# Optimization experiments

Hardware: AMD Instinct MI355X
Metric: run time of the kernel (lower is better)

## Reference

```python
import jax, jax.numpy as jnp
import numpy as np

N = 50000
NEG_SLOPE = 0.2  # PyG GATConv default leaky_relu slope


def _gat_layer(x, src, dst, W, a_s, a_d, b):
    # x: [N, Fin]; W: [Fin, H*C]; a_s, a_d: [H, C]; b: [C]
    H, C = a_s.shape
    xp = (x @ W).reshape(N, H, C)                      # projected node features per head
    alpha_s = jnp.einsum('nhc,hc->nh', xp, a_s)        # [N, H]
    alpha_d = jnp.einsum('nhc,hc->nh', xp, a_d)        # [N, H]
    e = jax.nn.leaky_relu(alpha_s[src] + alpha_d[dst], NEG_SLOPE)  # [E, H]
    # segment softmax over incoming edges of each dst node
    m = jax.ops.segment_max(e, dst, num_segments=N)
    m = jnp.where(jnp.isfinite(m), m, 0.0)
    p = jnp.exp(e - jax.lax.stop_gradient(m)[dst])
    denom = jax.ops.segment_sum(p, dst, num_segments=N)
    alpha = p / denom[dst]                             # [E, H]
    # scatter-aggregate messages
    out = jax.ops.segment_sum(alpha[:, :, None] * xp[src], dst, num_segments=N)  # [N, H, C]
    return out.mean(axis=1) + b                        # concat=False -> mean over heads


def setup_inputs() -> dict:
    key = jax.random.key(0)
    ks = jax.random.split(key, 16)
    IN, HID, OUT, H = 128, 64, 40, 4
    E = 800000
    x = jax.random.normal(ks[0], (N, IN), dtype=jnp.float32)
    edge_index = jax.random.randint(ks[1], (2, E), 0, N, dtype=jnp.int64)

    def mk(kw, ka, fin, fout):
        s = 1.0 / np.sqrt(fin)
        W = jax.random.normal(kw, (fin, H * fout), dtype=jnp.float32) * s
        a_s = jax.random.normal(ka, (H, fout), dtype=jnp.float32) * 0.1
        a_d = jax.random.normal(jax.random.fold_in(ka, 1), (H, fout), dtype=jnp.float32) * 0.1
        b = jnp.zeros((fout,), dtype=jnp.float32)
        return W, a_s, a_d, b

    W1, as1, ad1, b1 = mk(ks[2], ks[3], IN, HID)
    W2, as2, ad2, b2 = mk(ks[4], ks[5], HID, HID)
    W3, as3, ad3, b3 = mk(ks[6], ks[7], HID, OUT)
    return dict(x=x, edge_index=edge_index,
                W1=W1, as1=as1, ad1=ad1, b1=b1,
                W2=W2, as2=as2, ad2=ad2, b2=b2,
                W3=W3, as3=as3, ad3=ad3, b3=b3)


def reference(x, edge_index, W1, as1, ad1, b1, W2, as2, ad2, b2, W3, as3, ad3, b3):
    # PyG GATConv adds self-loops by default
    loop = jnp.arange(N, dtype=edge_index.dtype)
    src = jnp.concatenate([edge_index[0], loop])
    dst = jnp.concatenate([edge_index[1], loop])
    h = jax.nn.relu(_gat_layer(x, src, dst, W1, as1, ad1, b1))   # dropout is identity in eval
    h = jax.nn.relu(_gat_layer(h, src, dst, W2, as2, ad2, b2))
    h = jax.nn.relu(_gat_layer(h, src, dst, W3, as3, ad3, b3))
    return jax.nn.log_softmax(h, axis=-1)
```

## Files before the change

kernel.cpp:

```cpp
#include <hip/hip_runtime.h>
#include <math.h>

#define NNODES 50000
#define NEG_SLOPE 0.2f

typedef unsigned short ushort8v __attribute__((ext_vector_type(8)));
typedef unsigned short ushort4v __attribute__((ext_vector_type(4)));
typedef short short8v __attribute__((ext_vector_type(8)));
typedef float f32x4 __attribute__((ext_vector_type(4)));

__device__ __forceinline__ float lrelu(float x){ return x > 0.f ? x : NEG_SLOPE * x; }
__device__ __forceinline__ float bf2f(unsigned short u){ return __uint_as_float(((unsigned)u) << 16); }
__device__ __forceinline__ unsigned short f2bf(float f){
    unsigned u = __float_as_uint(f);
    u += 0x7fff + ((u >> 16) & 1);
    return (unsigned short)(u >> 16);
}

__global__ void detect_kernel(const unsigned long long* __restrict__ e, int* __restrict__ flag){
    const unsigned long long v = e[threadIdx.x & 63];
    const unsigned long long mask = __ballot(v >= (1ULL << 32));
    if(threadIdx.x == 0) *flag = (mask == 0ULL) ? 1 : 0;
}

__global__ void convert_kernel(const void* __restrict__ e, const int* __restrict__ flag,
                               int* __restrict__ out, int* __restrict__ deg,
                               int total, int E){
    int i = blockIdx.x * blockDim.x + threadIdx.x;
    if(i < total){
        int v;
        if(*flag) v = (int)((const long long*)e)[i];
        else      v = ((const int*)e)[i];
        out[i] = v;
        if(i >= E) atomicAdd(&deg[v], 1);
    }
}

__global__ void f2bf_kernel(const float* __restrict__ in, unsigned short* __restrict__ out, int total4){
    const int i = blockIdx.x * blockDim.x + threadIdx.x;
    if(i < total4){
        const float4 v = *(const float4*)&in[(size_t)i * 4];
        ushort4v o;
        o[0] = f2bf(v.x); o[1] = f2bf(v.y); o[2] = f2bf(v.z); o[3] = f2bf(v.w);
        *(ushort4v*)&out[(size_t)i * 4] = o;
    }
}

__global__ void wt_kernel(const float* __restrict__ W, unsigned short* __restrict__ Wt, int K, int NC){
    const int i = blockIdx.x * blockDim.x + threadIdx.x;
    if(i < K * NC){
        const int n = i / K, k = i - n * K;
        Wt[i] = f2bf(W[(size_t)k * NC + n]);
    }
}

__global__ __launch_bounds__(512) void scan1_kernel(const int* __restrict__ deg,
                                                    int* __restrict__ excl,
                                                    int* __restrict__ bsum, int n){
    __shared__ int sh[512];
    const int t = threadIdx.x;
    const int gid = blockIdx.x * 512 + t;
    const int v = (gid < n) ? deg[gid] : 0;
    sh[t] = v;
    __syncthreads();
    for(int off = 1; off < 512; off <<= 1){
        const int add = (t >= off) ? sh[t - off] : 0;
        __syncthreads();
        sh[t] += add;
        __syncthreads();
    }
    if(gid < n) excl[gid] = sh[t] - v;
    if(t == 511) bsum[blockIdx.x] = sh[511];
}

__global__ __launch_bounds__(128) void scan2_kernel(int* __restrict__ bsum, int nb){
    __shared__ int sh[128];
    const int t = threadIdx.x;
    const int v = (t < nb) ? bsum[t] : 0;
    sh[t] = v;
    __syncthreads();
    for(int off = 1; off < 128; off <<= 1){
        const int add = (t >= off) ? sh[t - off] : 0;
        __syncthreads();
        sh[t] += add;
        __syncthreads();
    }
    if(t < nb) bsum[t] = sh[t] - v;
}

__global__ void scan3_kernel(const int* __restrict__ excl, const int* __restrict__ bsum,
                             int* __restrict__ row_ptr, int* __restrict__ cursor,
                             int n, int E){
    const int gid = blockIdx.x * blockDim.x + threadIdx.x;
    if(gid < n){
        const int r = excl[gid] + bsum[gid >> 9];
        row_ptr[gid] = r;
        cursor[gid] = r;
    }
    if(gid == 0) row_ptr[n] = E;
}

__global__ void scatter_kernel(const int* __restrict__ src, const int* __restrict__ dst,
                               int* __restrict__ cursor, int* __restrict__ col, int E){
    int i = blockIdx.x * blockDim.x + threadIdx.x;
    if(i < E){
        int d = dst[i];
        int pos = atomicAdd(&cursor[d], 1);
        col[pos] = src[i];
    }
}

template<int K, int NC>
__global__ __launch_bounds__(256) void mfma_gemm_kernel(const unsigned short* __restrict__ A,
                                                        const unsigned short* __restrict__ Bt,
                                                        unsigned short* __restrict__ C,
                                                        int M){
    const int lane = threadIdx.x & 63;
    const int wave = threadIdx.x >> 6;
    const int quad = lane >> 4;
    const int l16 = lane & 15;
    const int bm = blockIdx.x * 64;
    const int bn = blockIdx.y * 64;
    const int m = min(bm + wave * 16 + l16, M - 1);
    const size_t arow = (size_t)m * K;

    f32x4 acc[4] = {{0,0,0,0},{0,0,0,0},{0,0,0,0},{0,0,0,0}};
    int cn[4];
    #pragma unroll
    for(int t = 0; t < 4; t++) cn[t] = min(bn + t * 16 + l16, NC - 1);

    #pragma unroll
    for(int k0 = 0; k0 < K; k0 += 32){
        const short8v a = *(const short8v*)&A[arow + k0 + quad * 8];
        #pragma unroll
        for(int t = 0; t < 4; t++){
            const short8v b = *(const short8v*)&Bt[(size_t)cn[t] * K + k0 + quad * 8];
            acc[t] = __builtin_amdgcn_mfma_f32_16x16x32_bf16(a, b, acc[t], 0, 0, 0);
        }
    }
    const int rbase = bm + wave * 16 + quad * 4;
    #pragma unroll
    for(int t = 0; t < 4; t++){
        const int c = bn + t * 16 + l16;
        if(c < NC){
            #pragma unroll
            for(int r = 0; r < 4; r++){
                const int row = rbase + r;
                if(row < M) C[(size_t)row * NC + c] = f2bf(acc[t][r]);
            }
        }
    }
}

template<int HC, int C>
__global__ __launch_bounds__(256) void alpha_kernel(const unsigned short* __restrict__ xp,
                                                    const float* __restrict__ a_s,
                                                    const float* __restrict__ a_d,
                                                    float* __restrict__ aS,
                                                    float* __restrict__ aD){
    constexpr int LANES = HC / 8;
    constexpr int LPH = LANES / 4;
    __shared__ float sS[4][32];
    __shared__ float sD[4][32];
    const int wave = threadIdx.x >> 6;
    const int lane = threadIdx.x & 63;
    const int n = blockIdx.x * 4 + wave;
    float ps = 0.f, pd = 0.f;
    if(lane < LANES){
        const ushort8v v = *(const ushort8v*)&xp[(size_t)n * HC + 8 * lane];
        #pragma unroll
        for(int j = 0; j < 8; j++){
            const float f = bf2f(v[j]);
            ps += f * a_s[8 * lane + j];
            pd += f * a_d[8 * lane + j];
        }
        sS[wave][lane] = ps; sD[wave][lane] = pd;
    }
    __syncthreads();
    if(lane < 4){
        const int lo = lane * LPH;
        float ss = 0.f, dd = 0.f;
        for(int i = 0; i < LPH; i++){ ss += sS[wave][lo + i]; dd += sD[wave][lo + i]; }
        aS[n * 4 + lane] = ss;
        aD[n * 4 + lane] = dd;
    }
}

template<int C, bool FINAL>
__global__ __launch_bounds__(256) void gather_kernel(const unsigned short* __restrict__ xp,
                                                     const int* __restrict__ row_ptr,
                                                     const int* __restrict__ col,
                                                     const float* __restrict__ aS,
                                                     const float* __restrict__ aD,
                                                     const float* __restrict__ bias,
                                                     void* __restrict__ outv){
    constexpr int HC = 4 * C;
    constexpr int LPE = HC / 8;
    __shared__ float sbuf[4][FINAL ? HC : 1];
    const int lane = threadIdx.x & 63;
    const int wave = threadIdx.x >> 6;
    const int n = blockIdx.x * 4 + wave;
    const int half = lane >> 5;
    const int hl = lane & 31;
    const bool active = hl < LPE;
    const int head = min((8 * hl) / C, 3);
    const int rs = row_ptr[n], re = row_ptr[n + 1];
    const int T = re - rs + 1;
    const float adh = aD[n * 4 + head];

    float acc[8] = {0,0,0,0,0,0,0,0};
    float denom = 0.f;
    int k = 0;
    for(; k + 4 <= T; k += 4){
        const int eA = rs + k + half;
        const int eB = eA + 2;
        const int sA = (eA < re) ? col[eA] : n;
        const int sB = (eB < re) ? col[eB] : n;
        const float avA = aS[(size_t)sA * 4 + head];
        const float avB = aS[(size_t)sB * 4 + head];
        const float wA = __expf(lrelu(avA + adh));
        const float wB = __expf(lrelu(avB + adh));
        denom += wA + wB;
        if(active){
            const ushort8v vA = *(const ushort8v*)&xp[(size_t)sA * HC + 8 * hl];
            const ushort8v vB = *(const ushort8v*)&xp[(size_t)sB * HC + 8 * hl];
            #pragma unroll
            for(int j = 0; j < 8; j++) acc[j] += wA * bf2f(vA[j]);
            #pragma unroll
            for(int j = 0; j < 8; j++) acc[j] += wB * bf2f(vB[j]);
        }
    }
    for(; k + 2 <= T; k += 2){
        const int e = rs + k + half;
        const int s = (e < re) ? col[e] : n;
        const float av = aS[(size_t)s * 4 + head];
        const float wh = __expf(lrelu(av + adh));
        denom += wh;
        if(active){
            const ushort8v v = *(const ushort8v*)&xp[(size_t)s * HC + 8 * hl];
            #pragma unroll
            for(int j = 0; j < 8; j++) acc[j] += wh * bf2f(v[j]);
        }
    }
    if(k < T && half == 0){
        const int e = rs + k;
        const int s = (e < re) ? col[e] : n;
        const float av = aS[(size_t)s * 4 + head];
        const float wh = __expf(lrelu(av + adh));
        denom += wh;
        if(active){
            const ushort8v v = *(const ushort8v*)&xp[(size_t)s * HC + 8 * hl];
            #pragma unroll
            for(int j = 0; j < 8; j++) acc[j] += wh * bf2f(v[j]);
        }
    }
    #pragma unroll
    for(int j = 0; j < 8; j++) acc[j] += __shfl_xor(acc[j], 32);
    denom += __shfl_xor(denom, 32);
    const float ih = 1.f / denom;
    #pragma unroll
    for(int j = 0; j < 8; j++) acc[j] *= ih;

    if(!FINAL){
        #pragma unroll
        for(int j = 0; j < 8; j++){
            acc[j] += __shfl_xor(acc[j], 8);
            acc[j] += __shfl_xor(acc[j], 16);
        }
        if(lane < 8){
            unsigned short* out = (unsigned short*)outv;
            ushort8v o;
            #pragma unroll
            for(int j = 0; j < 8; j++)
                o[j] = f2bf(fmaxf(acc[j] * 0.25f + bias[8 * lane + j], 0.f));
            *(ushort8v*)&out[(size_t)n * C + 8 * lane] = o;
        }
    } else {
        if(active && half == 0){
            #pragma unroll
            for(int j = 0; j < 8; j++) sbuf[wave][8 * hl + j] = acc[j];
        }
        __syncthreads();
        float* out = (float*)outv;
        float4 o = {0,0,0,0};
        if(lane < 10){
            const int c = 4 * lane;
            #pragma unroll
            for(int h = 0; h < 4; h++){
                o.x += sbuf[wave][h * 40 + c + 0];
                o.y += sbuf[wave][h * 40 + c + 1];
                o.z += sbuf[wave][h * 40 + c + 2];
                o.w += sbuf[wave][h * 40 + c + 3];
            }
            const float4 b4 = *(const float4*)&bias[c];
            o.x = fmaxf(o.x * 0.25f + b4.x, 0.f);
            o.y = fmaxf(o.y * 0.25f + b4.y, 0.f);
            o.z = fmaxf(o.z * 0.25f + b4.z, 0.f);
            o.w = fmaxf(o.w * 0.25f + b4.w, 0.f);
        }
        float lm = (lane < 10) ? fmaxf(fmaxf(o.x, o.y), fmaxf(o.z, o.w)) : -INFINITY;
        #pragma unroll
        for(int off = 8; off; off >>= 1) lm = fmaxf(lm, __shfl_xor(lm, off));
        float se = 0.f;
        if(lane < 10) se = __expf(o.x-lm) + __expf(o.y-lm) + __expf(o.z-lm) + __expf(o.w-lm);
        #pragma unroll
        for(int off = 8; off; off >>= 1) se += __shfl_xor(se, off);
        const float logZ = lm + logf(se);
        if(lane < 10){
            float4 r = {o.x - logZ, o.y - logZ, o.z - logZ, o.w - logZ};
            *(float4*)&out[(size_t)n * 40 + 4 * lane] = r;
        }
    }
}

extern "C" void kernel_launch(void* const* d_in, const int* in_sizes, int n_in,
                              void* d_out, int out_size, void* d_ws, size_t ws_size,
                              hipStream_t stream){
    const int N = NNODES;
    const int E = in_sizes[1] / 2;

    const float* x   = (const float*)d_in[0];
    const float* W1  = (const float*)d_in[2];
    const float* as1 = (const float*)d_in[3];
    const float* ad1 = (const float*)d_in[4];
    const float* b1  = (const float*)d_in[5];
    const float* W2  = (const float*)d_in[6];
    const float* as2 = (const float*)d_in[7];
    const float* ad2 = (const float*)d_in[8];
    const float* b2  = (const float*)d_in[9];
    const float* W3  = (const float*)d_in[10];
    const float* as3 = (const float*)d_in[11];
    const float* ad3 = (const float*)d_in[12];
    const float* b3  = (const float*)d_in[13];

    char* ws = (char*)d_ws;
    size_t off = 0;
    auto alloc = [&](size_t bytes) -> void* {
        void* p = ws + off;
        off = (off + bytes + 255) & ~(size_t)255;
        return p;
    };
    int*   flag    = (int*)  alloc(4);
    int*   e32     = (int*)  alloc((size_t)2 * E * 4);
    int*   row_ptr = (int*)  alloc((size_t)(N + 1) * 4);
    int*   colv    = (int*)  alloc((size_t)E * 4);
    int*   cursor  = (int*)  alloc((size_t)N * 4);
    int*   deg     = (int*)  alloc((size_t)N * 4);
    int*   excl    = (int*)  alloc((size_t)N * 4);
    int*   bsum    = (int*)  alloc(128 * 4);
    unsigned short* xp  = (unsigned short*)alloc((size_t)N * 256 * 2);
    unsigned short* xbf = (unsigned short*)alloc((size_t)N * 128 * 2);
    unsigned short* W1t = (unsigned short*)alloc((size_t)256 * 128 * 2);
    unsigned short* W2t = (unsigned short*)alloc((size_t)256 * 64 * 2);
    unsigned short* W3t = (unsigned short*)alloc((size_t)160 * 64 * 2);
    float* aS      = (float*)alloc((size_t)N * 4 * 4);
    float* aD      = (float*)alloc((size_t)N * 4 * 4);
    unsigned short* h = (unsigned short*)alloc((size_t)N * 64 * 2);
    (void)ws_size;

    hipMemsetAsync(deg, 0, (size_t)N * 4, stream);
    detect_kernel<<<1, 64, 0, stream>>>((const unsigned long long*)d_in[1], flag);
    convert_kernel<<<(2 * E + 255) / 256, 256, 0, stream>>>(d_in[1], flag, e32, deg, 2 * E, E);
    const int* srcv = e32;
    const int* dstv = e32 + E;

    f2bf_kernel<<<(N * 128 / 4 + 255) / 256, 256, 0, stream>>>(x, xbf, N * 128 / 4);
    wt_kernel<<<(128 * 256 + 255) / 256, 256, 0, stream>>>(W1, W1t, 128, 256);
    wt_kernel<<<(64 * 256 + 255) / 256, 256, 0, stream>>>(W2, W2t, 64, 256);
    wt_kernel<<<(64 * 160 + 255) / 256, 256, 0, stream>>>(W3, W3t, 64, 160);

    const int nbScan = (N + 511) / 512;
    scan1_kernel<<<nbScan, 512, 0, stream>>>(deg, excl, bsum, N);
    scan2_kernel<<<1, 128, 0, stream>>>(bsum, nbScan);
    scan3_kernel<<<(N + 255) / 256, 256, 0, stream>>>(excl, bsum, row_ptr, cursor, N, E);
    scatter_kernel<<<(E + 255) / 256, 256, 0, stream>>>(srcv, dstv, cursor, colv, E);

    const int nodeBlocks = N / 4;
    const int mBlocks = (N + 63) / 64;

    mfma_gemm_kernel<128, 256><<<dim3(mBlocks, 4), 256, 0, stream>>>(xbf, W1t, xp, N);
    alpha_kernel<256, 64><<<nodeBlocks, 256, 0, stream>>>(xp, as1, ad1, aS, aD);
    gather_kernel<64, false><<<nodeBlocks, 256, 0, stream>>>(xp, row_ptr, colv, aS, aD, b1, h);

    mfma_gemm_kernel<64, 256><<<dim3(mBlocks, 4), 256, 0, stream>>>(h, W2t, xp, N);
    alpha_kernel<256, 64><<<nodeBlocks, 256, 0, stream>>>(xp, as2, ad2, aS, aD);
    gather_kernel<64, false><<<nodeBlocks, 256, 0, stream>>>(xp, row_ptr, colv, aS, aD, b2, h);

    mfma_gemm_kernel<64, 160><<<dim3(mBlocks, 3), 256, 0, stream>>>(h, W3t, xp, N);
    alpha_kernel<160, 40><<<nodeBlocks, 256, 0, stream>>>(xp, as3, ad3, aS, aD);
    gather_kernel<40, true><<<nodeBlocks, 256, 0, stream>>>(xp, row_ptr, colv, aS, aD, b3, (float*)d_out);
}
```

Before: 477.3 us.

## Fold attention vectors into GEMM weights, precompute exp factors, drop alpha kernel

Extends each transposed weight matrix with eight extra columns (W·a_s and W·a_d per head), so the GEMM also produces the attention logits and the separate alpha kernel goes away. The GEMM now covers all output columns in one block per row tile, and its epilogue stores exp(v) and exp(0.2v) pairs. The gather can then form the edge weight as max of two products instead of calling exp per edge, and it uses packed two-wide float math for the bf16 accumulation. This skips the per-node max subtraction and relies on the exp values staying in range. Rounding the attention weights to bf16 also changes numerics slightly.

```diff
diff --git a/kernel.cpp b/kernel.cpp
--- a/kernel.cpp
+++ b/kernel.cpp
@@ -8,8 +8,8 @@
 typedef unsigned short ushort4v __attribute__((ext_vector_type(4)));
 typedef short short8v __attribute__((ext_vector_type(8)));
 typedef float f32x4 __attribute__((ext_vector_type(4)));
-
-__device__ __forceinline__ float lrelu(float x){ return x > 0.f ? x : NEG_SLOPE * x; }
+typedef float f32x2 __attribute__((ext_vector_type(2)));
+
 __device__ __forceinline__ float bf2f(unsigned short u){ return __uint_as_float(((unsigned)u) << 16); }
 __device__ __forceinline__ unsigned short f2bf(float f){
     unsigned u = __float_as_uint(f);
@@ -46,12 +46,34 @@
     }
 }
 
-__global__ void wt_kernel(const float* __restrict__ W, unsigned short* __restrict__ Wt, int K, int NC){
-    const int i = blockIdx.x * blockDim.x + threadIdx.x;
-    if(i < K * NC){
-        const int n = i / K, k = i - n * K;
-        Wt[i] = f2bf(W[(size_t)k * NC + n]);
-    }
+__device__ __forceinline__ void emit_wt(const float* __restrict__ W, const float* __restrict__ a_s,
+                                        const float* __restrict__ a_d, unsigned short* __restrict__ Wt,
+                                        int K, int NC, int C, int id){
+    const int n = id / K, k = id - n * K;
+    float v;
+    if(n < NC){
+        v = W[(size_t)k * NC + n];
+    } else {
+        const int h = n - NC;
+        const int hh = h & 3;
+        const float* av = (h < 4) ? a_s : a_d;
+        v = 0.f;
+        for(int c = 0; c < C; c++) v += W[(size_t)k * NC + hh * C + c] * av[hh * C + c];
+    }
+    Wt[(size_t)n * K + k] = f2bf(v);
+}
+
+__global__ void prep_kernel(const float* __restrict__ W1, const float* __restrict__ as1, const float* __restrict__ ad1,
+                            const float* __restrict__ W2, const float* __restrict__ as2, const float* __restrict__ ad2,
+                            const float* __restrict__ W3, const float* __restrict__ as3, const float* __restrict__ ad3,
+                            unsigned short* __restrict__ W1t, unsigned short* __restrict__ W2t,
+                            unsigned short* __restrict__ W3t){
+    int id = blockIdx.x * blockDim.x + threadIdx.x;
+    if(id < 264 * 128){ emit_wt(W1, as1, ad1, W1t, 128, 256, 64, id); return; }
+    id -= 264 * 128;
+    if(id < 264 * 64){ emit_wt(W2, as2, ad2, W2t, 64, 256, 64, id); return; }
+    id -= 264 * 64;
+    if(id < 168 * 64){ emit_wt(W3, as3, ad3, W3t, 64, 160, 40, id); }
 }
 
 __global__ __launch_bounds__(512) void scan1_kernel(const int* __restrict__ deg,
@@ -114,75 +136,55 @@
 __global__ __launch_bounds__(256) void mfma_gemm_kernel(const unsigned short* __restrict__ A,
                                                         const unsigned short* __restrict__ Bt,
                                                         unsigned short* __restrict__ C,
+                                                        f32x2* __restrict__ ea,
+                                                        f32x2* __restrict__ ed,
                                                         int M){
+    constexpr int NT = NC / 16 + 1;
     const int lane = threadIdx.x & 63;
     const int wave = threadIdx.x >> 6;
     const int quad = lane >> 4;
     const int l16 = lane & 15;
     const int bm = blockIdx.x * 64;
-    const int bn = blockIdx.y * 64;
     const int m = min(bm + wave * 16 + l16, M - 1);
     const size_t arow = (size_t)m * K;
 
-    f32x4 acc[4] = {{0,0,0,0},{0,0,0,0},{0,0,0,0},{0,0,0,0}};
-    int cn[4];
+    f32x4 acc[NT];
     #pragma unroll
-    for(int t = 0; t < 4; t++) cn[t] = min(bn + t * 16 + l16, NC - 1);
-
+    for(int t = 0; t < NT; t++) acc[t] = (f32x4){0,0,0,0};
+    int cn[NT];
     #pragma unroll
+    for(int t = 0; t < NT; t++) cn[t] = min(t * 16 + l16, NC + 7);
+
     for(int k0 = 0; k0 < K; k0 += 32){
         const short8v a = *(const short8v*)&A[arow + k0 + quad * 8];
         #pragma unroll
-        for(int t = 0; t < 4; t++){
+        for(int t = 0; t < NT; t++){
             const short8v b = *(const short8v*)&Bt[(size_t)cn[t] * K + k0 + quad * 8];
             acc[t] = __builtin_amdgcn_mfma_f32_16x16x32_bf16(a, b, acc[t], 0, 0, 0);
         }
     }
     const int rbase = bm + wave * 16 + quad * 4;
     #pragma unroll
-    for(int t = 0; t < 4; t++){
-        const int c = bn + t * 16 + l16;
-        if(c < NC){
-            #pragma unroll
-            for(int r = 0; r < 4; r++){
-                const int row = rbase + r;
-                if(row < M) C[(size_t)row * NC + c] = f2bf(acc[t][r]);
+    for(int t = 0; t < NT - 1; t++){
+        const int c = t * 16 + l16;
+        #pragma unroll
+        for(int r = 0; r < 4; r++){
+            const int row = rbase + r;
+            if(row < M) C[(size_t)row * NC + c] = f2bf(acc[t][r]);
+        }
+    }
+    if(l16 < 8){
+        const int h = l16 & 3;
+        f32x2* dst = (l16 < 4) ? ea : ed;
+        #pragma unroll
+        for(int r = 0; r < 4; r++){
+            const int row = rbase + r;
+            if(row < M){
+                const float v = acc[NT - 1][r];
+                f32x2 e2 = {__expf(v), __expf(NEG_SLOPE * v)};
+                dst[(size_t)row * 4 + h] = e2;
             }
         }
-    }
-}
-
-template<int HC, int C>
-__global__ __launch_bounds__(256) void alpha_kernel(const unsigned short* __restrict__ xp,
-                                                    const float* __restrict__ a_s,
-                                                    const float* __restrict__ a_d,
-                                                    float* __restrict__ aS,
-                                                    float* __restrict__ aD){
-    constexpr int LANES = HC / 8;
-    constexpr int LPH = LANES / 4;
-    __shared__ float sS[4][32];
-    __shared__ float sD[4][32];
-    const int wave = threadIdx.x >> 6;
-    const int lane = threadIdx.x & 63;
-    const int n = blockIdx.x * 4 + wave;
-    float ps = 0.f, pd = 0.f;
-    if(lane < LANES){
-        const ushort8v v = *(const ushort8v*)&xp[(size_t)n * HC + 8 * lane];
-        #pragma unroll
-        for(int j = 0; j < 8; j++){
-            const float f = bf2f(v[j]);
-            ps += f * a_s[8 * lane + j];
-            pd += f * a_d[8 * lane + j];
-        }
-        sS[wave][lane] = ps; sD[wave][lane] = pd;
-    }
-    __syncthreads();
-    if(lane < 4){
-        const int lo = lane * LPH;
-        float ss = 0.f, dd = 0.f;
-        for(int i = 0; i < LPH; i++){ ss += sS[wave][lo + i]; dd += sD[wave][lo + i]; }
-        aS[n * 4 + lane] = ss;
-        aD[n * 4 + lane] = dd;
     }
 }
 
@@ -190,8 +192,8 @@
 __global__ __launch_bounds__(256) void gather_kernel(const unsigned short* __restrict__ xp,
                                                      const int* __restrict__ row_ptr,
                                                      const int* __restrict__ col,
-                                                     const float* __restrict__ aS,
-                                                     const float* __restrict__ aD,
+                                                     const f32x2* __restrict__ ea,
+                                                     const f32x2* __restrict__ ed,
                                                      const float* __restrict__ bias,
                                                      void* __restrict__ outv){
     constexpr int HC = 4 * C;
@@ -206,9 +208,10 @@
     const int head = min((8 * hl) / C, 3);
     const int rs = row_ptr[n], re = row_ptr[n + 1];
     const int T = re - rs + 1;
-    const float adh = aD[n * 4 + head];
-
-    float acc[8] = {0,0,0,0,0,0,0,0};
+    const f32x2 edh = ed[(size_t)n * 4 + head];
+    const unsigned short* xpl = xp + 8 * hl;
+
+    f32x2 acc2[4] = {{0,0},{0,0},{0,0},{0,0}};
     float denom = 0.f;
     int k = 0;
     for(; k + 4 <= T; k += 4){
@@ -216,50 +219,66 @@
         const int eB = eA + 2;
         const int sA = (eA < re) ? col[eA] : n;
         const int sB = (eB < re) ? col[eB] : n;
-        const float avA = aS[(size_t)sA * 4 + head];
-        const float avB = aS[(size_t)sB * 4 + head];
-        const float wA = __expf(lrelu(avA + adh));
-        const float wB = __expf(lrelu(avB + adh));
+        const f32x2 a2 = ea[(size_t)sA * 4 + head];
+        const f32x2 b2 = ea[(size_t)sB * 4 + head];
+        const float wA = fmaxf(a2[0] * edh[0], a2[1] * edh[1]);
+        const float wB = fmaxf(b2[0] * edh[0], b2[1] * edh[1]);
         denom += wA + wB;
         if(active){
-            const ushort8v vA = *(const ushort8v*)&xp[(size_t)sA * HC + 8 * hl];
-            const ushort8v vB = *(const ushort8v*)&xp[(size_t)sB * HC + 8 * hl];
-            #pragma unroll
-            for(int j = 0; j < 8; j++) acc[j] += wA * bf2f(vA[j]);
-            #pragma unroll
-            for(int j = 0; j < 8; j++) acc[j] += wB * bf2f(vB[j]);
+            const uint4 uA = *(const uint4*)&xpl[(size_t)sA * HC];
+            const uint4 uB = *(const uint4*)&xpl[(size_t)sB * HC];
+            const f32x2 wA2 = {wA, wA};
+            const f32x2 wB2 = {wB, wB};
+            acc2[0] += wA2 * (f32x2){__uint_as_float(uA.x << 16), __uint_as_float(uA.x & 0xffff0000u)};
+            acc2[1] += wA2 * (f32x2){__uint_as_float(uA.y << 16), __uint_as_float(uA.y & 0xffff0000u)};
+            acc2[2] += wA2 * (f32x2){__uint_as_float(uA.z << 16), __uint_as_float(uA.z & 0xffff0000u)};
+            acc2[3] += wA2 * (f32x2){__uint_as_float(uA.w << 16), __uint_as_float(uA.w & 0xffff0000u)};
+            acc2[0] += wB2 * (f32x2){__uint_as_float(uB.x << 16), __uint_as_float(uB.x & 0xffff0000u)};
+            acc2[1] += wB2 * (f32x2){__uint_as_float(uB.y << 16), __uint_as_float(uB.y & 0xffff0000u)};
+            acc2[2] += wB2 * (f32x2){__uint_as_float(uB.z << 16), __uint_as_float(uB.z & 0xffff0000u)};
+            acc2[3] += wB2 * (f32x2){__uint_as_float(uB.w << 16), __uint_as_float(uB.w & 0xffff0000u)};
         }
     }
     for(; k + 2 <= T; k += 2){
         const int e = rs + k + half;
         const int s = (e < re) ? col[e] : n;
-        const float av = aS[(size_t)s * 4 + head];
-        const float wh = __expf(lrelu(av + adh));
+        const f32x2 a2 = ea[(size_t)s * 4 + head];
+        const float wh = fmaxf(a2[0] * edh[0], a2[1] * edh[1]);
         denom += wh;
         if(active){
-            const ushort8v v = *(const ushort8v*)&xp[(size_t)s * HC + 8 * hl];
-            #pragma unroll
-            for(int j = 0; j < 8; j++) acc[j] += wh * bf2f(v[j]);
+            const uint4 u = *(const uint4*)&xpl[(size_t)s * HC];
+            const f32x2 w2 = {wh, wh};
+            acc2[0] += w2 * (f32x2){__uint_as_float(u.x << 16), __uint_as_float(u.x & 0xffff0000u)};
+            acc2[1] += w2 * (f32x2){__uint_as_float(u.y << 16), __uint_as_float(u.y & 0xffff0000u)};
+            acc2[2] += w2 * (f32x2){__uint_as_float(u.z << 16), __uint_as_float(u.z & 0xffff0000u)};
+            acc2[3] += w2 * (f32x2){__uint_as_float(u.w << 16), __uint_as_float(u.w & 0xffff0000u)};
         }
     }
     if(k < T && half == 0){
         const int e = rs + k;
         const int s = (e < re) ? col[e] : n;
-        const float av = aS[(size_t)s * 4 + head];
-        const float wh = __expf(lrelu(av + adh));
+        const f32x2 a2 = ea[(size_t)s * 4 + head];
+        const float wh = fmaxf(a2[0] * edh[0], a2[1] * edh[1]);
         denom += wh;
         if(active){
-            const ushort8v v = *(const ushort8v*)&xp[(size_t)s * HC + 8 * hl];
-            #pragma unroll
-            for(int j = 0; j < 8; j++) acc[j] += wh * bf2f(v[j]);
+            const uint4 u = *(const uint4*)&xpl[(size_t)s * HC];
+            const f32x2 w2 = {wh, wh};
+            acc2[0] += w2 * (f32x2){__uint_as_float(u.x << 16), __uint_as_float(u.x & 0xffff0000u)};
+            acc2[1] += w2 * (f32x2){__uint_as_float(u.y << 16), __uint_as_float(u.y & 0xffff0000u)};
+            acc2[2] += w2 * (f32x2){__uint_as_float(u.z << 16), __uint_as_float(u.z & 0xffff0000u)};
+            acc2[3] += w2 * (f32x2){__uint_as_float(u.w << 16), __uint_as_float(u.w & 0xffff0000u)};
         }
     }
     #pragma unroll
-    for(int j = 0; j < 8; j++) acc[j] += __shfl_xor(acc[j], 32);
+    for(int p = 0; p < 4; p++){
+        acc2[p][0] += __shfl_xor(acc2[p][0], 32);
+        acc2[p][1] += __shfl_xor(acc2[p][1], 32);
+    }
     denom += __shfl_xor(denom, 32);
     const float ih = 1.f / denom;
+    float acc[8];
     #pragma unroll
-    for(int j = 0; j < 8; j++) acc[j] *= ih;
+    for(int p = 0; p < 4; p++){ acc[2*p] = acc2[p][0] * ih; acc[2*p+1] = acc2[p][1] * ih; }
 
     if(!FINAL){
         #pragma unroll
@@ -350,11 +369,11 @@
     int*   bsum    = (int*)  alloc(128 * 4);
     unsigned short* xp  = (unsigned short*)alloc((size_t)N * 256 * 2);
     unsigned short* xbf = (unsigned short*)alloc((size_t)N * 128 * 2);
-    unsigned short* W1t = (unsigned short*)alloc((size_t)256 * 128 * 2);
-    unsigned short* W2t = (unsigned short*)alloc((size_t)256 * 64 * 2);
-    unsigned short* W3t = (unsigned short*)alloc((size_t)160 * 64 * 2);
-    float* aS      = (float*)alloc((size_t)N * 4 * 4);
-    float* aD      = (float*)alloc((size_t)N * 4 * 4);
+    unsigned short* W1t = (unsigned short*)alloc((size_t)264 * 128 * 2);
+    unsigned short* W2t = (unsigned short*)alloc((size_t)264 * 64 * 2);
+    unsigned short* W3t = (unsigned short*)alloc((size_t)168 * 64 * 2);
+    f32x2* eav     = (f32x2*)alloc((size_t)N * 4 * 8);
+    f32x2* edv     = (f32x2*)alloc((size_t)N * 4 * 8);
     unsigned short* h = (unsigned short*)alloc((size_t)N * 64 * 2);
     (void)ws_size;
 
@@ -365,9 +384,9 @@
     const int* dstv = e32 + E;
 
     f2bf_kernel<<<(N * 128 / 4 + 255) / 256, 256, 0, stream>>>(x, xbf, N * 128 / 4);
-    wt_kernel<<<(128 * 256 + 255) / 256, 256, 0, stream>>>(W1, W1t, 128, 256);
-    wt_kernel<<<(64 * 256 + 255) / 256, 256, 0, stream>>>(W2, W2t, 64, 256);
-    wt_kernel<<<(64 * 160 + 255) / 256, 256, 0, stream>>>(W3, W3t, 64, 160);
+    const int prepTotal = 264 * 128 + 264 * 64 + 168 * 64;
+    prep_kernel<<<(prepTotal + 255) / 256, 256, 0, stream>>>(W1, as1, ad1, W2, as2, ad2,
+                                                             W3, as3, ad3, W1t, W2t, W3t);
 
     const int nbScan = (N + 511) / 512;
     scan1_kernel<<<nbScan, 512, 0, stream>>>(deg, excl, bsum, N);
@@ -378,15 +397,12 @@
     const int nodeBlocks = N / 4;
     const int mBlocks = (N + 63) / 64;
 
-    mfma_gemm_kernel<128, 256><<<dim3(mBlocks, 4), 256, 0, stream>>>(xbf, W1t, xp, N);
-    alpha_kernel<256, 64><<<nodeBlocks, 256, 0, stream>>>(xp, as1, ad1, aS, aD);
-    gather_kernel<64, false><<<nodeBlocks, 256, 0, stream>>>(xp, row_ptr, colv, aS, aD, b1, h);
-
-    mfma_gemm_kernel<64, 256><<<dim3(mBlocks, 4), 256, 0, stream>>>(h, W2t, xp, N);
-    alpha_kernel<256, 64><<<nodeBlocks, 256, 0, stream>>>(xp, as2, ad2, aS, aD);
-    gather_kernel<64, false><<<nodeBlocks, 256, 0, stream>>>(xp, row_ptr, colv, aS, aD, b2, h);
-
-    mfma_gemm_kernel<64, 160><<<dim3(mBlocks, 3), 256, 0, stream>>>(h, W3t, xp, N);
-    alpha_kernel<160, 40><<<nodeBlocks, 256, 0, stream>>>(xp, as3, ad3, aS, aD);
-    gather_kernel<40, true><<<nodeBlocks, 256, 0, stream>>>(xp, row_ptr, colv, aS, aD, b3, (float*)d_out);
-}
+    mfma_gemm_kernel<128, 256><<<mBlocks, 256, 0, stream>>>(xbf, W1t, xp, eav, edv, N);
+    gather_kernel<64, false><<<nodeBlocks, 256, 0, stream>>>(xp, row_ptr, colv, eav, edv, b1, h);
+
+    mfma_gemm_kernel<64, 256><<<mBlocks, 256, 0, stream>>>(h, W2t, xp, eav, edv, N);
+    gather_kernel<64, false><<<nodeBlocks, 256, 0, stream>>>(xp, row_ptr, colv, eav, edv, b2, h);
+
+    mfma_gemm_kernel<64, 160><<<mBlocks, 256, 0, stream>>>(h, W3t, xp, eav, edv, N);
+    gather_kernel<40, true><<<nodeBlocks, 256, 0, stream>>>(xp, row_ptr, colv, eav, edv, b3, (float*)d_out);
+}
```

New measurement: 483.2 us. About the same (+1.2%).
